# Optimization experiments

Measured on AMD Instinct MI355X. Metric: run time of the kernel, lower is better.

The kernel has to match this reference:

```python
import jax, jax.numpy as jnp
import numpy as np

N = 1_000_000
D_IN = 57   # hardcoded reshape(1,57) in original aggregate()
D_OUT = 128
K = 3       # num_sample=3 hardcoded in _get_unique_neighs_list


def _masked_mean_aggregate(h, neigh_idx, neigh_mask):
    # h: [N, D]; neigh_idx: [N, K] int; neigh_mask: [N, K] {0,1}
    feats = h[neigh_idx]                                   # [N, K, D] gather
    m = neigh_mask.astype(h.dtype)[..., None]              # [N, K, 1]
    s = jnp.sum(feats * m, axis=1)                         # [N, D]
    cnt = jnp.maximum(jnp.sum(neigh_mask, axis=1, keepdims=True).astype(h.dtype), 1.0)
    return s / cnt                                         # mask.mm(embed_matrix) equivalent (segment mean)


def _sage_layer(self_feats, aggregate_feats, W):
    # combined = cat([self, agg], dim=1); relu(W @ combined^T)^T; L2 normalize
    combined = jnp.concatenate([self_feats, aggregate_feats], axis=1)  # [N, 2D]
    out = jax.nn.relu(combined @ W.T)                                  # [N, out]
    norm = jnp.linalg.norm(out, axis=-1, keepdims=True)
    return out / jnp.maximum(norm, 1e-12)                              # F.normalize p=2 eps=1e-12


def setup_inputs() -> dict:
    key = jax.random.key(0)
    ks = jax.random.split(key, 7)
    x = jax.random.normal(ks[0], (N, D_IN), dtype=jnp.float32)
    W1 = jax.random.normal(ks[1], (D_OUT, 2 * D_IN), dtype=jnp.float32) * 0.1
    W2 = jax.random.normal(ks[2], (D_OUT, 2 * D_OUT), dtype=jnp.float32) * 0.1
    neigh_idx1 = jax.random.randint(ks[3], (N, K), 0, N, dtype=jnp.int32)
    neigh_mask1 = jax.random.randint(ks[4], (N, K), 0, 2, dtype=jnp.int32)
    neigh_idx2 = jax.random.randint(ks[5], (N, K), 0, N, dtype=jnp.int32)
    neigh_mask2 = jax.random.randint(ks[6], (N, K), 0, 2, dtype=jnp.int32)
    return {"x": x, "W1": W1, "W2": W2,
            "neigh_idx1": neigh_idx1, "neigh_mask1": neigh_mask1,
            "neigh_idx2": neigh_idx2, "neigh_mask2": neigh_mask2}


def reference(x, W1, W2, neigh_idx1, neigh_mask1, neigh_idx2, neigh_mask2):
    # Layer 1: aggregate over sampled neighbors of raw features, then SageLayer
    agg1 = _masked_mean_aggregate(x, neigh_idx1, neigh_mask1)
    h1 = _sage_layer(x, agg1, W1)                 # [N, D_OUT]
    # Layer 2
    agg2 = _masked_mean_aggregate(h1, neigh_idx2, neigh_mask2)
    h2 = _sage_layer(h1, agg2, W2)                # [N, D_OUT]
    return h2
```

## Files before the change

### kernel.cpp

```cpp
#include <hip/hip_runtime.h>
#include <hip/hip_bf16.h>

#define NN 1000000
#define NG 15625

typedef short bf16x8 __attribute__((ext_vector_type(8)));
typedef float f32x4  __attribute__((ext_vector_type(4)));
typedef unsigned short u16x8 __attribute__((ext_vector_type(8)));
typedef unsigned short u16x4 __attribute__((ext_vector_type(4)));

__device__ __forceinline__ float bf2f(unsigned short u){
  unsigned int x = ((unsigned int)u) << 16; float f;
  __builtin_memcpy(&f, &x, 4); return f;
}
__device__ __forceinline__ short f2bf(float v){
  __hip_bfloat16 h = __float2bfloat16(v); short s;
  __builtin_memcpy(&s, &h, 2); return s;
}

__global__ __launch_bounds__(512, 2) void sage2_mfma(
    const unsigned short* __restrict__ h1, const float* __restrict__ W2,
    const int* __restrict__ nidx, const int* __restrict__ nmask,
    float* __restrict__ out)
{
  __shared__ unsigned short comb[2][64 * 256];
  __shared__ float red[64][8];
  const int t   = threadIdx.x;
  const int l   = t & 63;
  const int w   = t >> 6;
  const int cfr = l & 15;
  const int kg  = l >> 4;

  bf16x8 Bf[8];
  #pragma unroll
  for (int ks = 0; ks < 8; ++ks) {
    const int col = w*16 + cfr;
    const float* p = W2 + col*256 + ks*32 + kg*8;
    f32x4 a = *reinterpret_cast<const f32x4*>(p);
    f32x4 b = *reinterpret_cast<const f32x4*>(p + 4);
    bf16x8 v;
    v[0]=f2bf(a[0]); v[1]=f2bf(a[1]); v[2]=f2bf(a[2]); v[3]=f2bf(a[3]);
    v[4]=f2bf(b[0]); v[5]=f2bf(b[1]); v[6]=f2bf(b[2]); v[7]=f2bf(b[3]);
    Bf[ks] = v;
  }

  const u16x8* hp = reinterpret_cast<const u16x8*>(h1);

  int nib0[2], nib1[2], nib2[2], nmb0[2], nmb1[2], nmb2[2];
  u16x8 sS[2], s0[2], s1[2], s2[2];
  float m0[2], m1[2], m2[2], iv[2];

  auto IDX = [&](int g){
    const long gb = (long)g * 64;
    #pragma unroll
    for (int i = 0; i < 2; ++i) {
      int n = (t + i*512) >> 4;
      long node = gb + n;
      nib0[i] = nidx[node*3+0]; nib1[i] = nidx[node*3+1]; nib2[i] = nidx[node*3+2];
      nmb0[i] = nmask[node*3+0]; nmb1[i] = nmask[node*3+1]; nmb2[i] = nmask[node*3+2];
    }
  };
  auto GATHER = [&](int g){
    const long gb = (long)g * 64;
    #pragma unroll
    for (int i = 0; i < 2; ++i) {
      int it = t + i*512;
      int n = it >> 4, q = it & 15;
      long node = gb + n;
      int b0 = nmb0[i], b1 = nmb1[i], b2 = nmb2[i];
      m0[i]=(float)b0; m1[i]=(float)b1; m2[i]=(float)b2;
      int c = b0+b1+b2; iv[i] = 1.0f/(float)(c<1?1:c);
      u16x8 z = {};
      sS[i] = hp[node*16 + q];
      s0[i] = b0 ? hp[(long)nib0[i]*16 + q] : z;
      s1[i] = b1 ? hp[(long)nib1[i]*16 + q] : z;
      s2[i] = b2 ? hp[(long)nib2[i]*16 + q] : z;
    }
  };
  auto UNPACK = [&](int p){
    char* cb = reinterpret_cast<char*>(comb[p]);
    #pragma unroll
    for (int i = 0; i < 2; ++i) {
      int it = t + i*512;
      int n = it >> 4, q = it & 15;
      int sw = (n & 7) << 4;
      *reinterpret_cast<u16x8*>(cb + n*512 + ((q*16) ^ sw)) = sS[i];
      u16x8 r;
      #pragma unroll
      for (int j = 0; j < 8; ++j)
        r[j] = (unsigned short)f2bf(
            (m0[i]*bf2f(s0[i][j]) + m1[i]*bf2f(s1[i][j]) + m2[i]*bf2f(s2[i][j])) * iv[i]);
      *reinterpret_cast<u16x8*>(cb + n*512 + ((256 + q*16) ^ sw)) = r;
    }
  };

  const int g0 = blockIdx.x;
  IDX(g0); GATHER(g0);
  if (g0 + (int)gridDim.x < NG) IDX(g0 + gridDim.x);

  int p = 0;
  for (int g = g0; g < NG; g += gridDim.x) {
    const long gb = (long)g * 64;
    UNPACK(p);
    __syncthreads();

    int g1 = g + gridDim.x, g2 = g + 2*gridDim.x;
    if (g1 < NG) GATHER(g1);
    if (g2 < NG) IDX(g2);

    f32x4 acc[4];
    #pragma unroll
    for (int r = 0; r < 4; ++r) acc[r] = (f32x4){0.f,0.f,0.f,0.f};
    const int swz = (cfr & 7) << 4;
    char* cbp = reinterpret_cast<char*>(comb[p]);
    #pragma unroll
    for (int r = 0; r < 4; ++r) {
      const int rb = (r*16 + cfr) * 512;
      #pragma unroll
      for (int ks = 0; ks < 8; ++ks) {
        bf16x8 af = *reinterpret_cast<const bf16x8*>(cbp + rb + ((ks*64 + kg*16) ^ swz));
        acc[r] = __builtin_amdgcn_mfma_f32_16x16x32_bf16(af, Bf[ks], acc[r], 0,0,0);
      }
    }

    float ssv[4][4];
    #pragma unroll
    for (int r = 0; r < 4; ++r) {
      #pragma unroll
      for (int e = 0; e < 4; ++e) {
        float v = fmaxf(acc[r][e], 0.f); acc[r][e] = v;
        float s = v*v;
        s += __shfl_xor(s, 1); s += __shfl_xor(s, 2);
        s += __shfl_xor(s, 4); s += __shfl_xor(s, 8);
        ssv[r][e] = s;
      }
      if (cfr < 4) {
        float v = cfr==0 ? ssv[r][0] : cfr==1 ? ssv[r][1] : cfr==2 ? ssv[r][2] : ssv[r][3];
        red[r*16 + kg*4 + cfr][w] = v;
      }
    }
    __syncthreads();

    #pragma unroll
    for (int r = 0; r < 4; ++r) {
      #pragma unroll
      for (int e = 0; e < 4; ++e) {
        int row = r*16 + kg*4 + e;
        f32x4 ra = *reinterpret_cast<const f32x4*>(&red[row][0]);
        f32x4 rb = *reinterpret_cast<const f32x4*>(&red[row][4]);
        float tot = (ra[0]+ra[1]) + (ra[2]+ra[3]) + (rb[0]+rb[1]) + (rb[2]+rb[3]);
        float inv = 1.0f / fmaxf(sqrtf(tot), 1e-12f);
        __builtin_nontemporal_store(acc[r][e] * inv,
                                    &out[(gb + row)*128 + w*16 + cfr]);
      }
    }
    p ^= 1;
  }
}

__global__ __launch_bounds__(256, 2) void sage1_mfma(
    const float* __restrict__ x, const float* __restrict__ W1,
    const int* __restrict__ nidx, const int* __restrict__ nmask,
    unsigned short* __restrict__ h1)
{
  __shared__ unsigned short comb[64 * 128];
  __shared__ float red[64][4];
  const int t   = threadIdx.x;
  const int l   = t & 63;
  const int w   = t >> 6;
  const int cfr = l & 15;
  const int kg  = l >> 4;

  bf16x8 Bf[4][2];
  #pragma unroll
  for (int ks = 0; ks < 4; ++ks) {
    #pragma unroll
    for (int nf = 0; nf < 2; ++nf) {
      const int col = w*32 + nf*16 + cfr;
      const int k0  = ks*32 + kg*8;
      bf16x8 v;
      #pragma unroll
      for (int j = 0; j < 8; ++j) {
        int lk = k0 + j;
        int wk = lk < 64 ? lk : lk - 7;
        bool valid = (lk < 57) || (lk >= 64 && lk < 121);
        v[j] = valid ? f2bf(W1[col*114 + wk]) : (short)0;
      }
      Bf[ks][nf] = v;
    }
  }

  char* cb = reinterpret_cast<char*>(comb);

  f32x4 sf[4], n0[4], n1[4], n2[4];
  float m0[4], m1[4], m2[4], iv[4];

  auto ISSUE = [&](int g){
    const long gb = (long)g * 64;
    #pragma unroll
    for (int i = 0; i < 4; ++i) {
      int it = t + i*256;
      int n = it >> 4, q = it & 15;
      long node = gb + n;
      int j0 = nidx[node*3+0], j1 = nidx[node*3+1], j2 = nidx[node*3+2];
      int b0 = nmask[node*3+0], b1 = nmask[node*3+1], b2 = nmask[node*3+2];
      m0[i]=(float)b0; m1[i]=(float)b1; m2[i]=(float)b2;
      int c = b0+b1+b2; iv[i] = 1.0f/(float)(c<1?1:c);
      #pragma unroll
      for (int jj = 0; jj < 4; ++jj) {
        int j = q*4 + jj;
        bool jv = j < 57;
        sf[i][jj] = jv         ? x[node*57 + j]     : 0.f;
        n0[i][jj] = (b0 && jv) ? x[(long)j0*57 + j] : 0.f;
        n1[i][jj] = (b1 && jv) ? x[(long)j1*57 + j] : 0.f;
        n2[i][jj] = (b2 && jv) ? x[(long)j2*57 + j] : 0.f;
      }
    }
  };

  if (blockIdx.x < NG) ISSUE(blockIdx.x);

  for (int g = blockIdx.x; g < NG; g += gridDim.x) {
    const long gb = (long)g * 64;
    #pragma unroll
    for (int i = 0; i < 4; ++i) {
      int it = t + i*256;
      int n = it >> 4, q = it & 15;
      int sw = (n & 7) << 4;
      u16x4 vs, va;
      #pragma unroll
      for (int jj = 0; jj < 4; ++jj) {
        vs[jj] = (unsigned short)f2bf(sf[i][jj]);
        va[jj] = (unsigned short)f2bf(
            (m0[i]*n0[i][jj] + m1[i]*n1[i][jj] + m2[i]*n2[i][jj]) * iv[i]);
      }
      *reinterpret_cast<u16x4*>(cb + n*256 + ((q*8) ^ sw))       = vs;
      *reinterpret_cast<u16x4*>(cb + n*256 + ((128 + q*8) ^ sw)) = va;
    }
    __syncthreads();

    int gn = g + gridDim.x;
    if (gn < NG) ISSUE(gn);

    f32x4 acc[4][2];
    #pragma unroll
    for (int r = 0; r < 4; ++r) {
      acc[r][0] = (f32x4){0.f,0.f,0.f,0.f};
      acc[r][1] = (f32x4){0.f,0.f,0.f,0.f};
    }
    const int swz = (cfr & 7) << 4;
    #pragma unroll
    for (int r = 0; r < 4; ++r) {
      const int rb = (r*16 + cfr) * 256;
      #pragma unroll
      for (int ks = 0; ks < 4; ++ks) {
        bf16x8 af = *reinterpret_cast<const bf16x8*>(cb + rb + ((ks*64 + kg*16) ^ swz));
        acc[r][0] = __builtin_amdgcn_mfma_f32_16x16x32_bf16(af, Bf[ks][0], acc[r][0], 0,0,0);
        acc[r][1] = __builtin_amdgcn_mfma_f32_16x16x32_bf16(af, Bf[ks][1], acc[r][1], 0,0,0);
      }
    }

    float ssv[4][4];
    #pragma unroll
    for (int r = 0; r < 4; ++r) {
      #pragma unroll
      for (int e = 0; e < 4; ++e) {
        float v0 = fmaxf(acc[r][0][e], 0.f); acc[r][0][e] = v0;
        float v1 = fmaxf(acc[r][1][e], 0.f); acc[r][1][e] = v1;
        float s = v0*v0 + v1*v1;
        s += __shfl_xor(s, 1); s += __shfl_xor(s, 2);
        s += __shfl_xor(s, 4); s += __shfl_xor(s, 8);
        ssv[r][e] = s;
      }
      if (cfr < 4) {
        float v = cfr==0 ? ssv[r][0] : cfr==1 ? ssv[r][1] : cfr==2 ? ssv[r][2] : ssv[r][3];
        red[r*16 + kg*4 + cfr][w] = v;
      }
    }
    __syncthreads();

    #pragma unroll
    for (int r = 0; r < 4; ++r) {
      #pragma unroll
      for (int e = 0; e < 4; ++e) {
        int row = r*16 + kg*4 + e;
        float tot = red[row][0] + red[row][1] + red[row][2] + red[row][3];
        float inv = 1.0f / fmaxf(sqrtf(tot), 1e-12f);
        long node = gb + row;
        h1[node*128 + w*32 + cfr]      = (unsigned short)f2bf(acc[r][0][e] * inv);
        h1[node*128 + w*32 + 16 + cfr] = (unsigned short)f2bf(acc[r][1][e] * inv);
      }
    }
  }
}

extern "C" void kernel_launch(void* const* d_in, const int* in_sizes, int n_in,
                              void* d_out, int out_size, void* d_ws, size_t ws_size,
                              hipStream_t stream) {
  const float* x   = (const float*)d_in[0];
  const float* W1  = (const float*)d_in[1];
  const float* W2  = (const float*)d_in[2];
  const int* idx1  = (const int*)d_in[3];
  const int* msk1  = (const int*)d_in[4];
  const int* idx2  = (const int*)d_in[5];
  const int* msk2  = (const int*)d_in[6];
  float* out = (float*)d_out;
  unsigned short* h1 = (unsigned short*)d_ws;

  sage1_mfma<<<2048, 256, 0, stream>>>(x, W1, idx1, msk1, h1);
  sage2_mfma<<<512,  512, 0, stream>>>(h1, W2, idx2, msk2, out);
}
```

Measured before the change: 743.5 us.

## Stream self features via direct-to-LDS loads and vectorize layer-1 gathers

In layer 2, the self-feature rows of h1 now go straight into a double-buffered LDS tile through global_load_lds. They no longer pass through registers and the unpack step, which saves VGPRs and VALU stores. The aggregate half is held in its own single LDS buffer, and the MFMA loop is split into self and aggregate passes. Layer 1 swaps the per-element scalar x loads for 16-byte vector loads, handles the 57th column separately, and zeroes the padding columns once at the start instead of rewriting them on every tile. The layer-2 output store also becomes a normal store in place of a nontemporal one.

```diff
diff --git a/kernel.cpp b/kernel.cpp
--- a/kernel.cpp
+++ b/kernel.cpp
@@ -23,7 +23,8 @@
     const int* __restrict__ nidx, const int* __restrict__ nmask,
     float* __restrict__ out)
 {
-  __shared__ unsigned short comb[2][64 * 256];
+  __shared__ unsigned short selfS[2][64 * 128];
+  __shared__ unsigned short aggS[64 * 128];
   __shared__ float red[64][8];
   const int t   = threadIdx.x;
   const int l   = t & 63;
@@ -47,79 +48,94 @@
   const u16x8* hp = reinterpret_cast<const u16x8*>(h1);
 
   int nib0[2], nib1[2], nib2[2], nmb0[2], nmb1[2], nmb2[2];
-  u16x8 sS[2], s0[2], s1[2], s2[2];
+  u16x8 s0[2], s1[2], s2[2];
   float m0[2], m1[2], m2[2], iv[2];
 
   auto IDX = [&](int g){
     const long gb = (long)g * 64;
     #pragma unroll
     for (int i = 0; i < 2; ++i) {
-      int n = (t + i*512) >> 4;
-      long node = gb + n;
+      int nn = (t + i*512) >> 4;
+      long node = gb + nn;
       nib0[i] = nidx[node*3+0]; nib1[i] = nidx[node*3+1]; nib2[i] = nidx[node*3+2];
       nmb0[i] = nmask[node*3+0]; nmb1[i] = nmask[node*3+1]; nmb2[i] = nmask[node*3+2];
     }
   };
   auto GATHER = [&](int g){
-    const long gb = (long)g * 64;
     #pragma unroll
     for (int i = 0; i < 2; ++i) {
       int it = t + i*512;
-      int n = it >> 4, q = it & 15;
-      long node = gb + n;
+      int qq = it & 15;
       int b0 = nmb0[i], b1 = nmb1[i], b2 = nmb2[i];
       m0[i]=(float)b0; m1[i]=(float)b1; m2[i]=(float)b2;
       int c = b0+b1+b2; iv[i] = 1.0f/(float)(c<1?1:c);
       u16x8 z = {};
-      sS[i] = hp[node*16 + q];
-      s0[i] = b0 ? hp[(long)nib0[i]*16 + q] : z;
-      s1[i] = b1 ? hp[(long)nib1[i]*16 + q] : z;
-      s2[i] = b2 ? hp[(long)nib2[i]*16 + q] : z;
-    }
-  };
-  auto UNPACK = [&](int p){
-    char* cb = reinterpret_cast<char*>(comb[p]);
+      s0[i] = b0 ? hp[(long)nib0[i]*16 + qq] : z;
+      s1[i] = b1 ? hp[(long)nib1[i]*16 + qq] : z;
+      s2[i] = b2 ? hp[(long)nib2[i]*16 + qq] : z;
+    }
+  };
+  auto SELF_DMA = [&](int g, int pp){
     #pragma unroll
     for (int i = 0; i < 2; ++i) {
       int it = t + i*512;
-      int n = it >> 4, q = it & 15;
-      int sw = (n & 7) << 4;
-      *reinterpret_cast<u16x8*>(cb + n*512 + ((q*16) ^ sw)) = sS[i];
+      int nn = it >> 4, qq0 = it & 15;
+      long node = (long)g * 64 + nn;
+      int qq = qq0 ^ (nn & 7);
+      const unsigned short* gp = h1 + node*128 + qq*8;
+      unsigned short* lp = &selfS[pp][it*8];
+      __builtin_amdgcn_global_load_lds(
+          (const __attribute__((address_space(1))) unsigned short*)gp,
+          (__attribute__((address_space(3))) unsigned short*)lp, 16, 0, 0);
+    }
+  };
+  char* aggB = reinterpret_cast<char*>(aggS);
+  auto UNPACK_AGG = [&](){
+    #pragma unroll
+    for (int i = 0; i < 2; ++i) {
+      int it = t + i*512;
+      int nn = it >> 4, qq = it & 15;
+      int sw = (nn & 7) << 4;
       u16x8 r;
       #pragma unroll
       for (int j = 0; j < 8; ++j)
         r[j] = (unsigned short)f2bf(
             (m0[i]*bf2f(s0[i][j]) + m1[i]*bf2f(s1[i][j]) + m2[i]*bf2f(s2[i][j])) * iv[i]);
-      *reinterpret_cast<u16x8*>(cb + n*512 + ((256 + q*16) ^ sw)) = r;
+      *reinterpret_cast<u16x8*>(aggB + nn*256 + ((qq*16) ^ sw)) = r;
     }
   };
 
   const int g0 = blockIdx.x;
-  IDX(g0); GATHER(g0);
+  IDX(g0); GATHER(g0); SELF_DMA(g0, 0);
   if (g0 + (int)gridDim.x < NG) IDX(g0 + gridDim.x);
 
   int p = 0;
   for (int g = g0; g < NG; g += gridDim.x) {
     const long gb = (long)g * 64;
-    UNPACK(p);
+    UNPACK_AGG();
     __syncthreads();
 
     int g1 = g + gridDim.x, g2 = g + 2*gridDim.x;
-    if (g1 < NG) GATHER(g1);
+    if (g1 < NG) { GATHER(g1); SELF_DMA(g1, p ^ 1); }
     if (g2 < NG) IDX(g2);
 
     f32x4 acc[4];
     #pragma unroll
     for (int r = 0; r < 4; ++r) acc[r] = (f32x4){0.f,0.f,0.f,0.f};
     const int swz = (cfr & 7) << 4;
-    char* cbp = reinterpret_cast<char*>(comb[p]);
-    #pragma unroll
-    for (int r = 0; r < 4; ++r) {
-      const int rb = (r*16 + cfr) * 512;
-      #pragma unroll
-      for (int ks = 0; ks < 8; ++ks) {
-        bf16x8 af = *reinterpret_cast<const bf16x8*>(cbp + rb + ((ks*64 + kg*16) ^ swz));
+    char* selfB = reinterpret_cast<char*>(selfS) + p*(64*256);
+    #pragma unroll
+    for (int r = 0; r < 4; ++r) {
+      const int rb = (r*16 + cfr) * 256;
+      #pragma unroll
+      for (int ks = 0; ks < 4; ++ks) {
+        bf16x8 af = *reinterpret_cast<const bf16x8*>(selfB + rb + ((ks*64 + kg*16) ^ swz));
         acc[r] = __builtin_amdgcn_mfma_f32_16x16x32_bf16(af, Bf[ks], acc[r], 0,0,0);
+      }
+      #pragma unroll
+      for (int ks = 0; ks < 4; ++ks) {
+        bf16x8 af = *reinterpret_cast<const bf16x8*>(aggB + rb + ((ks*64 + kg*16) ^ swz));
+        acc[r] = __builtin_amdgcn_mfma_f32_16x16x32_bf16(af, Bf[ks + 4], acc[r], 0,0,0);
       }
     }
 
@@ -147,11 +163,10 @@
       for (int e = 0; e < 4; ++e) {
         int row = r*16 + kg*4 + e;
         f32x4 ra = *reinterpret_cast<const f32x4*>(&red[row][0]);
-        f32x4 rb = *reinterpret_cast<const f32x4*>(&red[row][4]);
-        float tot = (ra[0]+ra[1]) + (ra[2]+ra[3]) + (rb[0]+rb[1]) + (rb[2]+rb[3]);
+        f32x4 rb4 = *reinterpret_cast<const f32x4*>(&red[row][4]);
+        float tot = (ra[0]+ra[1]) + (ra[2]+ra[3]) + (rb4[0]+rb4[1]) + (rb4[2]+rb4[3]);
         float inv = 1.0f / fmaxf(sqrtf(tot), 1e-12f);
-        __builtin_nontemporal_store(acc[r][e] * inv,
-                                    &out[(gb + row)*128 + w*16 + cfr]);
+        out[(gb + row)*128 + w*16 + cfr] = acc[r][e] * inv;
       }
     }
     p ^= 1;
@@ -192,6 +207,14 @@
 
   char* cb = reinterpret_cast<char*>(comb);
 
+  for (int e = t; e < 128; e += 256) {
+    int nn = e >> 1, h = e & 1;
+    int chunk = h ? 15 : 7;
+    int u = chunk ^ (nn & 7);
+    *reinterpret_cast<u16x4*>(cb + nn*256 + u*16 + 8) = (u16x4){0,0,0,0};
+  }
+  __syncthreads();
+
   f32x4 sf[4], n0[4], n1[4], n2[4];
   float m0[4], m1[4], m2[4], iv[4];
 
@@ -200,20 +223,24 @@
     #pragma unroll
     for (int i = 0; i < 4; ++i) {
       int it = t + i*256;
-      int n = it >> 4, q = it & 15;
-      long node = gb + n;
+      int nn = it >> 4, qq = it & 15;
+      long node = gb + nn;
       int j0 = nidx[node*3+0], j1 = nidx[node*3+1], j2 = nidx[node*3+2];
       int b0 = nmask[node*3+0], b1 = nmask[node*3+1], b2 = nmask[node*3+2];
       m0[i]=(float)b0; m1[i]=(float)b1; m2[i]=(float)b2;
       int c = b0+b1+b2; iv[i] = 1.0f/(float)(c<1?1:c);
-      #pragma unroll
-      for (int jj = 0; jj < 4; ++jj) {
-        int j = q*4 + jj;
-        bool jv = j < 57;
-        sf[i][jj] = jv         ? x[node*57 + j]     : 0.f;
-        n0[i][jj] = (b0 && jv) ? x[(long)j0*57 + j] : 0.f;
-        n1[i][jj] = (b1 && jv) ? x[(long)j1*57 + j] : 0.f;
-        n2[i][jj] = (b2 && jv) ? x[(long)j2*57 + j] : 0.f;
+      f32x4 z = {0.f,0.f,0.f,0.f};
+      sf[i]=z; n0[i]=z; n1[i]=z; n2[i]=z;
+      if (qq < 14) {
+        __builtin_memcpy(&sf[i], x + node*57 + qq*4, 16);
+        if (b0) __builtin_memcpy(&n0[i], x + (long)j0*57 + qq*4, 16);
+        if (b1) __builtin_memcpy(&n1[i], x + (long)j1*57 + qq*4, 16);
+        if (b2) __builtin_memcpy(&n2[i], x + (long)j2*57 + qq*4, 16);
+      } else if (qq == 14) {
+        sf[i][0] = x[node*57 + 56];
+        if (b0) n0[i][0] = x[(long)j0*57 + 56];
+        if (b1) n1[i][0] = x[(long)j1*57 + 56];
+        if (b2) n2[i][0] = x[(long)j2*57 + 56];
       }
     }
   };
@@ -225,17 +252,19 @@
     #pragma unroll
     for (int i = 0; i < 4; ++i) {
       int it = t + i*256;
-      int n = it >> 4, q = it & 15;
-      int sw = (n & 7) << 4;
-      u16x4 vs, va;
-      #pragma unroll
-      for (int jj = 0; jj < 4; ++jj) {
-        vs[jj] = (unsigned short)f2bf(sf[i][jj]);
-        va[jj] = (unsigned short)f2bf(
-            (m0[i]*n0[i][jj] + m1[i]*n1[i][jj] + m2[i]*n2[i][jj]) * iv[i]);
-      }
-      *reinterpret_cast<u16x4*>(cb + n*256 + ((q*8) ^ sw))       = vs;
-      *reinterpret_cast<u16x4*>(cb + n*256 + ((128 + q*8) ^ sw)) = va;
+      int nn = it >> 4, qq = it & 15;
+      if (qq < 15) {
+        int sw = (nn & 7) << 4;
+        u16x4 vs, va;
+        #pragma unroll
+        for (int jj = 0; jj < 4; ++jj) {
+          vs[jj] = (unsigned short)f2bf(sf[i][jj]);
+          va[jj] = (unsigned short)f2bf(
+              (m0[i]*n0[i][jj] + m1[i]*n1[i][jj] + m2[i]*n2[i][jj]) * iv[i]);
+        }
+        *reinterpret_cast<u16x4*>(cb + nn*256 + ((qq*8) ^ sw))       = vs;
+        *reinterpret_cast<u16x4*>(cb + nn*256 + ((128 + qq*8) ^ sw)) = va;
+      }
     }
     __syncthreads();
 
```

After: 809.1 us. 8.8% more time.
